# Kernel tuning notes

Hardware: AMD Instinct MI355X
Metric: run time of the kernel (lower is better)

Reference implementation:

```python
import jax, jax.numpy as jnp
import numpy as np

N = 1_000_000        # points
V = 200_000          # occupied voxels
B = 4                # scans per batch
NUM_CLASSES = 20
DIM_POINT = 4
EPS = 1e-5


def bn(x, g, b):
    # eval-mode BatchNorm1d with running_mean=0, running_var=1
    return x * (g / jnp.sqrt(1.0 + EPS)) + b


def _lin(key, fi, fo):
    # kaiming-normal init, bias-free Linear stored as [in, out]
    return jax.random.normal(key, (fi, fo), jnp.float32) * np.sqrt(2.0 / fi)


def setup_inputs() -> dict:
    key = jax.random.key(0)
    ks = jax.random.split(key, 20)
    batch_ids = (jnp.arange(N) * B // N).astype(jnp.float32)[:, None]
    coords = jax.random.normal(ks[0], (N, DIM_POINT), jnp.float32)
    points = jnp.concatenate([batch_ids, coords], axis=1)           # [N, 1+dim_point]
    pv_ids = jax.random.randint(ks[1], (N,), 0, V, jnp.int64)       # point -> voxel
    ones, zeros = jnp.ones, jnp.zeros
    return {
        'points': points, 'point_voxel_ids': pv_ids,
        # point encoder: 4->32->64->32, each Linear(no bias)+BN+ReLU
        'pe_w1': _lin(ks[2], DIM_POINT, 32), 'pe_g1': ones(32), 'pe_b1': zeros(32),
        'pe_w2': _lin(ks[3], 32, 64),        'pe_g2': ones(64), 'pe_b2': zeros(64),
        'pe_w3': _lin(ks[4], 64, 32),        'pe_g3': ones(32), 'pe_b3': zeros(32),
        # voxel encoder (SparseUnet simplified to per-voxel 32->32->32)
        've_w1': _lin(ks[5], 32, 32), 've_g1': ones(32), 've_b1': zeros(32),
        've_w2': _lin(ks[6], 32, 32), 've_g2': ones(32), 've_b2': zeros(32),
        # fusion encoder: 64->64
        'fu_w': _lin(ks[7], 64, 64), 'fu_g': ones(64), 'fu_b': zeros(64),
        # FlattenSELayer: 64 -> 64//16 -> 64 with biases
        'se_w1': _lin(ks[8], 64, 4),  'se_b1': zeros(4),
        'se_w2': _lin(ks[9], 4, 64),  'se_b2': zeros(64),
        # main classifier 64->32->num_classes
        'cls_w1': _lin(ks[10], 64, 32), 'cls_g1': ones(32), 'cls_b1': zeros(32),
        'cls_w2': _lin(ks[11], 32, NUM_CLASSES),
        # aux classifier 32->32->num_classes
        'aux_w1': _lin(ks[12], 32, 32), 'aux_g1': ones(32), 'aux_b1': zeros(32),
        'aux_w2': _lin(ks[13], 32, NUM_CLASSES),
    }


def reference(points, point_voxel_ids,
              pe_w1, pe_g1, pe_b1, pe_w2, pe_g2, pe_b2, pe_w3, pe_g3, pe_b3,
              ve_w1, ve_g1, ve_b1, ve_w2, ve_g2, ve_b2,
              fu_w, fu_g, fu_b, se_w1, se_b1, se_w2, se_b2,
              cls_w1, cls_g1, cls_b1, cls_w2,
              aux_w1, aux_g1, aux_b1, aux_w2):
    batch_ids = points[:, 0].astype(jnp.int32)
    pv = point_voxel_ids.astype(jnp.int32)
    x = points[:, 1:]
    # point encoder
    pf = jax.nn.relu(bn(x @ pe_w1, pe_g1, pe_b1))
    pf = jax.nn.relu(bn(pf @ pe_w2, pe_g2, pe_b2))
    pf = jax.nn.relu(bn(pf @ pe_w3, pe_g3, pe_b3))               # [N,32]
    # voxel_max_pooling: point -> voxel scatter-max (empty voxels -> 0)
    vox = jax.ops.segment_max(pf, pv, num_segments=V)
    vox = jnp.where(jnp.isfinite(vox), vox, 0.0)                 # [V,32]
    # voxel encoder (SparseUnet stand-in); v1 is the aux feature tap
    v1 = jax.nn.relu(bn(vox @ ve_w1, ve_g1, ve_b1))              # [V,32]
    vf = jax.nn.relu(bn(v1 @ ve_w2, ve_g2, ve_b2))               # [V,32]
    # voxel_to_point gather + fusion
    pvf = vf[pv]                                                  # [N,32]
    fused = jnp.concatenate([pvf, pf], axis=1)                   # [N,64]
    fused = jax.nn.relu(bn(fused @ fu_w, fu_g, fu_b))
    # FlattenSELayer: per-scan mean -> gate -> residual scale
    sums = jax.ops.segment_sum(fused, batch_ids, num_segments=B)
    cnts = jax.ops.segment_sum(jnp.ones((fused.shape[0], 1), fused.dtype), batch_ids, num_segments=B)
    mean = sums / jnp.maximum(cnts, 1.0)                         # [B,64]
    gate = jax.nn.sigmoid(jax.nn.relu(mean @ se_w1 + se_b1) @ se_w2 + se_b2)
    fused = fused + fused * gate[batch_ids]
    # heads (dropout is identity at inference)
    out = jax.nn.relu(bn(fused @ cls_w1, cls_g1, cls_b1)) @ cls_w2      # [N,C]
    aux_out = jax.nn.relu(bn(v1 @ aux_w1, aux_g1, aux_b1)) @ aux_w2     # [V,C]
    return out, aux_out
```

## Files before the change

kernel.cpp:

```cpp
#include <hip/hip_runtime.h>
#include <hip/hip_bf16.h>

#define NPTS 1000000
#define NVOX 200000
#define NCLS 20

typedef __hip_bfloat16 bf16;
typedef __attribute__((ext_vector_type(8))) short bf16x8_t;
typedef __attribute__((ext_vector_type(4))) float f32x4_t;
#define MFMA16(a, b, c) __builtin_amdgcn_mfma_f32_16x16x32_bf16(a, b, c, 0, 0, 0)

constexpr size_t L_PTSC = 0;
constexpr size_t L_PV   = L_PTSC + (size_t)NPTS * 4;
constexpr size_t L_BID  = L_PV + NPTS;
constexpr size_t L_CNT  = L_BID + NPTS;
constexpr size_t L_BSUM = L_CNT + NVOX;
constexpr size_t L_BCNT = L_BSUM + 2048;
constexpr size_t L_GATE = L_BCNT + 4;
constexpr size_t L_FLAG = L_GATE + 256;
constexpr size_t L_OFFS = L_FLAG + 4;
constexpr size_t L_OFFW = L_OFFS + NVOX;
constexpr size_t L_BS1  = L_OFFW + NVOX;
constexpr size_t L_BB   = L_BS1 + 256;
constexpr size_t L_IDX  = L_BB + 256;
constexpr size_t L_W    = L_IDX + NPTS;
constexpr int O_PE1W = 0;      constexpr int O_PE1B = 128;
constexpr int O_PE2W = 160;    constexpr int O_PE2B = 2208;
constexpr int O_PE3W = 2272;   constexpr int O_PE3B = 4320;
constexpr int O_VE1W = 4352;   constexpr int O_VE1B = 5376;
constexpr int O_VE2W = 5408;   constexpr int O_VE2B = 6432;
constexpr int O_FUW  = 6464;   constexpr int O_FUB  = 10560;
constexpr int O_SE1W = 10624;  constexpr int O_SE1B = 10880;
constexpr int O_SE2W = 10884;  constexpr int O_SE2B = 11140;
constexpr int O_CLS1W = 11204; constexpr int O_CLS1B = 13252;
constexpr int O_CLS2W = 13284;
constexpr int O_AUX1W = 13924; constexpr int O_AUX1B = 14948;
constexpr int O_AUX2W = 14980;
constexpr int W_TOTAL = 15620;
constexpr size_t L_WT  = L_W + W_TOTAL;
static_assert((L_WT * 4) % 16 == 0, "WT alignment");
constexpr int WT_FU = 0;
constexpr int WT_C1 = 4096;
constexpr int WT_C2 = 6144;
constexpr int WT_2H = 7168;
constexpr int WT_2L = 9216;
constexpr int WT_3H = 11264;
constexpr int WT_3L = 13312;
constexpr int WT_U16 = 15360;
constexpr size_t L_VFU = L_WT + WT_U16 / 2;
constexpr size_t L_PFQ = L_VFU + (size_t)NVOX * 16;
constexpr size_t L_PFS = L_PFQ + (size_t)NPTS * 16;
static_assert((L_VFU * 4) % 16 == 0, "vf alignment");
static_assert((L_PFQ * 4) % 16 == 0, "pf alignment");
static_assert((L_PFS * 4) % 16 == 0, "pfs alignment");

static __device__ __forceinline__ float b2f(bf16 v) { return __bfloat162float(v); }
static __device__ __forceinline__ float us2f(unsigned short u) { return __uint_as_float((unsigned)u << 16); }
static __device__ __forceinline__ unsigned short f2us(float f) {
    unsigned u = __float_as_uint(f);
    u += 0x7fffu + ((u >> 16) & 1u);
    return (unsigned short)(u >> 16);
}
static __device__ __forceinline__ unsigned pack2(float a, float b) {
    return (unsigned)f2us(a) | ((unsigned)f2us(b) << 16);
}
static __device__ __forceinline__ void unpack2(unsigned u, float& a, float& b) {
    a = __uint_as_float(u << 16);
    b = __uint_as_float(u & 0xffff0000u);
}
static __device__ __forceinline__ float rdf(const void* p, size_t idx, int fp32) {
    return fp32 ? ((const float*)p)[idx] : b2f(((const bf16*)p)[idx]);
}
static __device__ __forceinline__ int detect_fp32(const void* pts_raw) {
    const unsigned short* ptsu = (const unsigned short*)pts_raw;
    return (ptsu[1] == 0 && ptsu[11] == 0) ? 1 : 0;
}
static __device__ __forceinline__ int detect_i64(const void* pv_raw) {
    const unsigned* pvu = (const unsigned*)pv_raw;
    return (pvu[1] == 0 && pvu[3] == 0 && pvu[5] == 0 && pvu[7] == 0) ? 1 : 0;
}

template <int K, int M, bool RELU, bool BIAS>
static __device__ __forceinline__ void dense(const float* __restrict__ x, float* __restrict__ y,
                                             const float* __restrict__ w, const float* __restrict__ b) {
#pragma unroll
    for (int j = 0; j < M; ++j) {
        float a = BIAS ? b[j] : 0.f;
#pragma unroll
        for (int k = 0; k < K; ++k) a = fmaf(x[k], w[k * M + j], a);
        y[j] = RELU ? fmaxf(a, 0.f) : a;
    }
}

static __device__ __forceinline__ int block_excl_scan(int v, int t) {
    __shared__ int sh[2][256];
    int cur = 0;
    sh[0][t] = v; __syncthreads();
#pragma unroll
    for (int off = 1; off < 256; off <<= 1) {
        int val = sh[cur][t];
        if (t >= off) val += sh[cur][t - off];
        sh[cur ^ 1][t] = val; __syncthreads();
        cur ^= 1;
    }
    return sh[cur][t] - v;
}

struct WPtrs {
    const void *pe_w1, *pe_g1, *pe_b1, *pe_w2, *pe_g2, *pe_b2, *pe_w3, *pe_g3, *pe_b3;
    const void *ve_w1, *ve_g1, *ve_b1, *ve_w2, *ve_g2, *ve_b2;
    const void *fu_w, *fu_g, *fu_b;
    const void *se_w1, *se_b1, *se_w2, *se_b2;
    const void *cls_w1, *cls_g1, *cls_b1, *cls_w2;
    const void *aux_w1, *aux_g1, *aux_b1, *aux_w2;
};

static __device__ void foldw(float* d, const void* w, const void* g, int K, int M, int fp32) {
    const float INV = 0.9999950000374997f;
    for (int idx = threadIdx.x; idx < K * M; idx += 256)
        d[idx] = rdf(w, idx, fp32) * (rdf(g, idx % M, fp32) * INV);
}
static __device__ void cpv(float* d, const void* s, int n, int fp32) {
    for (int idx = threadIdx.x; idx < n; idx += 256) d[idx] = rdf(s, idx, fp32);
}

__global__ void k0_prep(WPtrs p, const void* __restrict__ pts_raw, float* __restrict__ W,
                        unsigned short* __restrict__ WT) {
    int f = detect_fp32(pts_raw);
    foldw(W + O_PE1W, p.pe_w1, p.pe_g1, 4, 32, f);   cpv(W + O_PE1B, p.pe_b1, 32, f);
    foldw(W + O_PE2W, p.pe_w2, p.pe_g2, 32, 64, f);  cpv(W + O_PE2B, p.pe_b2, 64, f);
    foldw(W + O_PE3W, p.pe_w3, p.pe_g3, 64, 32, f);  cpv(W + O_PE3B, p.pe_b3, 32, f);
    foldw(W + O_VE1W, p.ve_w1, p.ve_g1, 32, 32, f);  cpv(W + O_VE1B, p.ve_b1, 32, f);
    foldw(W + O_VE2W, p.ve_w2, p.ve_g2, 32, 32, f);  cpv(W + O_VE2B, p.ve_b2, 32, f);
    foldw(W + O_FUW,  p.fu_w,  p.fu_g,  64, 64, f);  cpv(W + O_FUB,  p.fu_b, 64, f);
    cpv(W + O_SE1W, p.se_w1, 256, f);  cpv(W + O_SE1B, p.se_b1, 4, f);
    cpv(W + O_SE2W, p.se_w2, 256, f);  cpv(W + O_SE2B, p.se_b2, 64, f);
    foldw(W + O_CLS1W, p.cls_w1, p.cls_g1, 64, 32, f); cpv(W + O_CLS1B, p.cls_b1, 32, f);
    cpv(W + O_CLS2W, p.cls_w2, 640, f);
    foldw(W + O_AUX1W, p.aux_w1, p.aux_g1, 32, 32, f); cpv(W + O_AUX1B, p.aux_b1, 32, f);
    cpv(W + O_AUX2W, p.aux_w2, 640, f);
    __syncthreads();
    unsigned short* wtfu = WT + WT_FU;
    unsigned short* wtc1 = WT + WT_C1;
    unsigned short* wtc2 = WT + WT_C2;
    unsigned short* wt2h = WT + WT_2H;
    unsigned short* wt2l = WT + WT_2L;
    unsigned short* wt3h = WT + WT_3H;
    unsigned short* wt3l = WT + WT_3L;
    for (int idx = threadIdx.x; idx < 4096; idx += 256) {
        int n = idx >> 6, k = idx & 63;
        wtfu[idx] = f2us(W[O_FUW + k * 64 + n]);
    }
    for (int idx = threadIdx.x; idx < 2048; idx += 256) {
        int n = idx >> 6, k = idx & 63;
        wtc1[idx] = f2us(W[O_CLS1W + k * 32 + n]);
    }
    for (int idx = threadIdx.x; idx < 1024; idx += 256) {
        int n = idx >> 5, k = idx & 31;
        wtc2[idx] = (n < NCLS) ? f2us(W[O_CLS2W + k * NCLS + n]) : (unsigned short)0;
    }
    for (int idx = threadIdx.x; idx < 2048; idx += 256) {
        int n = idx >> 5, k = idx & 31;
        float v = W[O_PE2W + k * 64 + n];
        unsigned short hi = f2us(v);
        wt2h[idx] = hi;
        wt2l[idx] = f2us(v - us2f(hi));
    }
    for (int idx = threadIdx.x; idx < 2048; idx += 256) {
        int n = idx >> 6, k = idx & 63;
        float v = W[O_PE3W + k * 32 + n];
        unsigned short hi = f2us(v);
        wt3h[idx] = hi;
        wt3l[idx] = f2us(v - us2f(hi));
    }
}

__global__ __launch_bounds__(256) void k_scan1(const int* __restrict__ cnt, int* __restrict__ bs) {
    int t = threadIdx.x;
    int base = blockIdx.x * 1024 + t * 4;
    int s = 0;
#pragma unroll
    for (int k = 0; k < 4; ++k) { int idx = base + k; if (idx < NVOX) s += cnt[idx]; }
    __shared__ int red[256];
    red[t] = s; __syncthreads();
    for (int off = 128; off > 0; off >>= 1) { if (t < off) red[t] += red[t + off]; __syncthreads(); }
    if (t == 0) bs[blockIdx.x] = red[0];
}

__global__ __launch_bounds__(256) void k_scan2(const int* __restrict__ bs, int* __restrict__ bb, int nb) {
    int t = threadIdx.x;
    int v = (t < nb) ? bs[t] : 0;
    int e = block_excl_scan(v, t);
    bb[t] = e;
}

__global__ __launch_bounds__(256) void k_scan3(const int* __restrict__ cnt, const int* __restrict__ bb,
                                               int* __restrict__ offs) {
    int t = threadIdx.x;
    int base = blockIdx.x * 1024 + t * 4;
    int c[4]; int s = 0;
#pragma unroll
    for (int k = 0; k < 4; ++k) { int idx = base + k; c[k] = (idx < NVOX) ? cnt[idx] : 0; s += c[k]; }
    int run = bb[blockIdx.x] + block_excl_scan(s, t);
#pragma unroll
    for (int k = 0; k < 4; ++k) {
        int idx = base + k;
        if (idx < NVOX) { offs[idx] = run; run += c[k]; }
    }
}

__global__ __launch_bounds__(256) void k1_fused(const void* __restrict__ pts_raw,
                                                const void* __restrict__ pv_raw,
                                                const float* __restrict__ W,
                                                const unsigned short* __restrict__ WT2H,
                                                const unsigned short* __restrict__ WT2L,
                                                const unsigned short* __restrict__ WT3H,
                                                const unsigned short* __restrict__ WT3L,
                                                int* __restrict__ pvN,
                                                int* __restrict__ bidN,
                                                int* __restrict__ cnt,
                                                float* __restrict__ bcnt,
                                                int* __restrict__ rank,
                                                uint4* __restrict__ pf_q) {
    __shared__ __align__(16) unsigned short hth[4][16][72];
    __shared__ __align__(16) unsigned short htl[4][16][72];
    __shared__ __align__(16) unsigned short pt[4][16][40];
    int t = threadIdx.x;
    int lane = t & 63, w = t >> 6;
    int m = lane & 15, quad = lane >> 4;
    int i0 = blockIdx.x * 256;
    int fp32 = detect_fp32(pts_raw), i64 = detect_i64(pv_raw);

    float w1[32], b1[8];
#pragma unroll
    for (int k = 0; k < 4; ++k)
#pragma unroll
        for (int j = 0; j < 8; ++j) w1[k * 8 + j] = W[O_PE1W + k * 32 + quad * 8 + j];
#pragma unroll
    for (int j = 0; j < 8; ++j) b1[j] = W[O_PE1B + quad * 8 + j];
    bf16x8_t b2h[4], b2l[4], b3h[2][2], b3l[2][2];
    float bias2[4], bias3[2];
#pragma unroll
    for (int tn = 0; tn < 4; ++tn) {
        b2h[tn] = *(const bf16x8_t*)(WT2H + (tn * 16 + m) * 32 + quad * 8);
        b2l[tn] = *(const bf16x8_t*)(WT2L + (tn * 16 + m) * 32 + quad * 8);
        bias2[tn] = W[O_PE2B + tn * 16 + m];
    }
#pragma unroll
    for (int tn = 0; tn < 2; ++tn) {
#pragma unroll
        for (int kh = 0; kh < 2; ++kh) {
            b3h[tn][kh] = *(const bf16x8_t*)(WT3H + (tn * 16 + m) * 64 + kh * 32 + quad * 8);
            b3l[tn][kh] = *(const bf16x8_t*)(WT3L + (tn * 16 + m) * 64 + kh * 32 + quad * 8);
        }
        bias3[tn] = W[O_PE3B + tn * 16 + m];
    }
    int nval = NPTS - i0; if (nval > 256) nval = 256;
    int ntiles = (nval - w * 64 >= 64) ? 4 : 0;

#pragma unroll 1
    for (int tt = 0; tt < ntiles; ++tt) {
        int rbase = i0 + w * 64 + tt * 16;
        int arow = rbase + m;
        float4 c;
        c.x = rdf(pts_raw, (size_t)arow * 5 + 1, fp32);
        c.y = rdf(pts_raw, (size_t)arow * 5 + 2, fp32);
        c.z = rdf(pts_raw, (size_t)arow * 5 + 3, fp32);
        c.w = rdf(pts_raw, (size_t)arow * 5 + 4, fp32);
        union { unsigned u[4]; bf16x8_t v; } ah, al;
#pragma unroll
        for (int p = 0; p < 4; ++p) {
            unsigned hu = 0, lu = 0;
#pragma unroll
            for (int s = 0; s < 2; ++s) {
                int j = 2 * p + s;
                float h = b1[j];
                h = fmaf(c.x, w1[0 * 8 + j], h);
                h = fmaf(c.y, w1[1 * 8 + j], h);
                h = fmaf(c.z, w1[2 * 8 + j], h);
                h = fmaf(c.w, w1[3 * 8 + j], h);
                h = fmaxf(h, 0.f);
                unsigned short hi = f2us(h);
                unsigned short lo = f2us(h - us2f(hi));
                hu |= (unsigned)hi << (16 * s);
                lu |= (unsigned)lo << (16 * s);
            }
            ah.u[p] = hu; al.u[p] = lu;
        }
#pragma unroll
        for (int tn = 0; tn < 4; ++tn) {
            f32x4_t acc = {0.f, 0.f, 0.f, 0.f};
            acc = MFMA16(ah.v, b2h[tn], acc);
            acc = MFMA16(ah.v, b2l[tn], acc);
            acc = MFMA16(al.v, b2h[tn], acc);
#pragma unroll
            for (int e = 0; e < 4; ++e) {
                float v = fmaxf(acc[e] + bias2[tn], 0.f);
                unsigned short hi = f2us(v);
                hth[w][quad * 4 + e][tn * 16 + m] = hi;
                htl[w][quad * 4 + e][tn * 16 + m] = f2us(v - us2f(hi));
            }
        }
        bf16x8_t x0h = *(const bf16x8_t*)&hth[w][m][quad * 8];
        bf16x8_t x1h = *(const bf16x8_t*)&hth[w][m][32 + quad * 8];
        bf16x8_t x0l = *(const bf16x8_t*)&htl[w][m][quad * 8];
        bf16x8_t x1l = *(const bf16x8_t*)&htl[w][m][32 + quad * 8];
#pragma unroll
        for (int tn = 0; tn < 2; ++tn) {
            f32x4_t acc = {0.f, 0.f, 0.f, 0.f};
            acc = MFMA16(x0h, b3h[tn][0], acc);
            acc = MFMA16(x1h, b3h[tn][1], acc);
            acc = MFMA16(x0h, b3l[tn][0], acc);
            acc = MFMA16(x1h, b3l[tn][1], acc);
            acc = MFMA16(x0l, b3h[tn][0], acc);
            acc = MFMA16(x1l, b3h[tn][1], acc);
#pragma unroll
            for (int e = 0; e < 4; ++e)
                pt[w][quad * 4 + e][tn * 16 + m] = f2us(fmaxf(acc[e] + bias3[tn], 0.f));
        }
        uint4 q = *(const uint4*)&pt[w][m][quad * 8];
        pf_q[(size_t)arow * 4 + quad] = q;
    }

    int i = i0 + t;
    bool valid = t < nval;
    int b = 0, rk = 0;
    if (valid) {
        b = (int)rdf(pts_raw, (size_t)i * 5, fp32);
        bidN[i] = b;
        int v = i64 ? (int)((const long long*)pv_raw)[i] : ((const int*)pv_raw)[i];
        pvN[i] = v;
        rk = atomicAdd(&cnt[v], 1);
    }
    __shared__ int sb0, sflag;
    if (t == 0) { sb0 = b; sflag = 1; }
    __syncthreads();
    if (valid && b != sb0) sflag = 0;
    __syncthreads();
    if (sflag) {
        if (t == 0) atomicAdd(&bcnt[sb0], (float)nval);
    } else if (valid) {
        atomicAdd(&bcnt[b], 1.f);
    }
    if (valid) rank[i] = rk;
}

__global__ __launch_bounds__(256) void k_scat(const int* __restrict__ pv,
                                              const int* __restrict__ rank,
                                              const int* __restrict__ offs,
                                              const uint4* __restrict__ pf_q,
                                              uint4* __restrict__ pf_s) {
    int tid = blockIdx.x * 256 + threadIdx.x;
    int i = tid >> 2, quad = tid & 3;
    if (i >= NPTS) return;
    int sp = offs[pv[i]] + rank[i];
    pf_s[(size_t)sp * 4 + quad] = pf_q[(size_t)i * 4 + quad];
}

__global__ __launch_bounds__(256) void k_voxmlp(const int* __restrict__ offs, const int* __restrict__ cnt,
                                                const uint4* __restrict__ pf_s,
                                                const float* __restrict__ W,
                                                const void* __restrict__ pts_raw,
                                                unsigned* __restrict__ vf_u,
                                                void* __restrict__ outbase) {
    int v = blockIdx.x * 256 + threadIdx.x;
    if (v >= NVOX) return;
    int of32 = detect_fp32(pts_raw);
    float mx[32];
#pragma unroll
    for (int c = 0; c < 32; ++c) mx[c] = 0.f;
    int s = offs[v], n = cnt[v];
    for (int p = 0; p < n; ++p) {
        size_t base = (size_t)(s + p) * 4;
#pragma unroll
        for (int t = 0; t < 4; ++t) {
            uint4 q = pf_s[base + t];
            float a, b;
            unpack2(q.x, a, b); mx[8*t+0] = fmaxf(mx[8*t+0], a); mx[8*t+1] = fmaxf(mx[8*t+1], b);
            unpack2(q.y, a, b); mx[8*t+2] = fmaxf(mx[8*t+2], a); mx[8*t+3] = fmaxf(mx[8*t+3], b);
            unpack2(q.z, a, b); mx[8*t+4] = fmaxf(mx[8*t+4], a); mx[8*t+5] = fmaxf(mx[8*t+5], b);
            unpack2(q.w, a, b); mx[8*t+6] = fmaxf(mx[8*t+6], a); mx[8*t+7] = fmaxf(mx[8*t+7], b);
        }
    }
    float v1[32], vf[32], a1[32], o[20];
    dense<32, 32, true, true>(mx, v1, W + O_VE1W, W + O_VE1B);
    dense<32, 32, true, true>(v1, vf, W + O_VE2W, W + O_VE2B);
#pragma unroll
    for (int c = 0; c < 16; ++c) vf_u[(size_t)v * 16 + c] = pack2(vf[2*c], vf[2*c+1]);
    dense<32, 32, true, true>(v1, a1, W + O_AUX1W, W + O_AUX1B);
    dense<32, 20, false, false>(a1, o, W + O_AUX2W, nullptr);
    if (of32) {
        float* auxf = (float*)outbase + (size_t)NPTS * NCLS + (size_t)v * NCLS;
#pragma unroll
        for (int t = 0; t < NCLS; ++t) auxf[t] = o[t];
    } else {
        unsigned* auxu = (unsigned*)((bf16*)outbase + (size_t)NPTS * NCLS);
#pragma unroll
        for (int t = 0; t < 10; ++t) auxu[(size_t)v * 10 + t] = pack2(o[2*t], o[2*t+1]);
    }
}

__global__ __launch_bounds__(256) void k3_mfma(const int* __restrict__ bid, const int* __restrict__ pv,
                                               const uint4* __restrict__ pf_q,
                                               const uint4* __restrict__ vf_q,
                                               const float* __restrict__ W,
                                               const unsigned short* __restrict__ WTfu,
                                               float* __restrict__ bsum8) {
    __shared__ int sbid[256];
    __shared__ float red[4][64];
    __shared__ int sflag;
    int t = threadIdx.x;
    int i0 = blockIdx.x * 256;
    int nval = NPTS - i0; if (nval > 256) nval = 256;
    if (t < nval) sbid[t] = bid[i0 + t];
    if (t == 0) sflag = (bid[i0] == bid[i0 + nval - 1]) ? 1 : 0;

    int lane = t & 63, w = t >> 6;
    int m = lane & 15, quad = lane >> 4;
    bf16x8_t bw0[4], bw1[4];
    float bias[4];
#pragma unroll
    for (int tn = 0; tn < 4; ++tn) {
        bw0[tn] = *(const bf16x8_t*)(WTfu + (tn * 16 + m) * 64 + quad * 8);
        bw1[tn] = *(const bf16x8_t*)(WTfu + (tn * 16 + m) * 64 + 32 + quad * 8);
        bias[tn] = W[O_FUB + tn * 16 + m];
    }
    __syncthreads();
    int uni = sflag;
    int b0 = sbid[0];
    int rep = (blockIdx.x & 7) * 256;
    int ntiles = (nval - w * 64 >= 64) ? 4 : 0;

    float csum[4] = {0.f, 0.f, 0.f, 0.f};
#pragma unroll
    for (int tt = 0; tt < 4; ++tt) {
        if (tt >= ntiles) break;
        int rbase = i0 + w * 64 + tt * 16;
        int arow = rbase + m;
        int pvr = pv[arow];
        uint4 va = vf_q[(size_t)pvr * 4 + quad];
        uint4 vb = pf_q[(size_t)arow * 4 + quad];
        bf16x8_t a0 = *(bf16x8_t*)&va;
        bf16x8_t a1 = *(bf16x8_t*)&vb;
        float f[4][4];
#pragma unroll
        for (int tn = 0; tn < 4; ++tn) {
            f32x4_t acc = {0.f, 0.f, 0.f, 0.f};
            acc = MFMA16(a0, bw0[tn], acc);
            acc = MFMA16(a1, bw1[tn], acc);
#pragma unroll
            for (int e = 0; e < 4; ++e) f[tn][e] = fmaxf(acc[e] + bias[tn], 0.f);
        }
        if (uni) {
#pragma unroll
            for (int tn = 0; tn < 4; ++tn) {
                float s = f[tn][0] + f[tn][1] + f[tn][2] + f[tn][3];
                s += __shfl_xor(s, 16);
                s += __shfl_xor(s, 32);
                csum[tn] += s;
            }
        } else {
#pragma unroll
            for (int tn = 0; tn < 4; ++tn)
#pragma unroll
                for (int e = 0; e < 4; ++e)
                    atomicAdd(&bsum8[rep + sbid[rbase - i0 + quad * 4 + e] * 64 + tn * 16 + m], f[tn][e]);
        }
    }
    if (uni) {
        float mine = quad == 0 ? csum[0] : quad == 1 ? csum[1] : quad == 2 ? csum[2] : csum[3];
        red[w][quad * 16 + m] = mine;
        __syncthreads();
        if (t < 64) {
            float s = red[0][t] + red[1][t] + red[2][t] + red[3][t];
            atomicAdd(&bsum8[rep + b0 * 64 + t], s);
        }
    }
}

__global__ void k4_gate(const float* __restrict__ bsum8, const float* __restrict__ bcnt,
                        const float* __restrict__ W, float* __restrict__ gate) {
    __shared__ float m[4][64];
    __shared__ float hid[4][4];
    int tid = threadIdx.x, b = tid >> 6, c = tid & 63;
    float s = 0.f;
#pragma unroll
    for (int r = 0; r < 8; ++r) s += bsum8[r * 256 + tid];
    m[b][c] = s / fmaxf(bcnt[b], 1.f);
    __syncthreads();
    if (c < 4) {
        const float* w = W + O_SE1W;
        float a = (W + O_SE1B)[c];
        for (int k = 0; k < 64; ++k) a = fmaf(m[b][k], w[k * 4 + c], a);
        hid[b][c] = fmaxf(a, 0.f);
    }
    __syncthreads();
    const float* w2 = W + O_SE2W;
    float g = (W + O_SE2B)[c];
#pragma unroll
    for (int h = 0; h < 4; ++h) g = fmaf(hid[b][h], w2[h * 64 + c], g);
    gate[tid] = 1.f + 1.f / (1.f + expf(-g));
}

__global__ __launch_bounds__(256) void k5_mfma(const int* __restrict__ bid, const int* __restrict__ pv,
                                               const uint4* __restrict__ pf_q,
                                               const uint4* __restrict__ vf_q,
                                               const float* __restrict__ W,
                                               const unsigned short* __restrict__ WTfu,
                                               const unsigned short* __restrict__ WTc1,
                                               const unsigned short* __restrict__ WTc2,
                                               const float* __restrict__ gate,
                                               const void* __restrict__ pts_raw,
                                               void* __restrict__ out) {
    __shared__ float sg[256];
    __shared__ int sbid[256];
    __shared__ int sflag;
    __shared__ __align__(16) unsigned short ft[4][16][72];
    __shared__ __align__(16) unsigned short ht[4][16][40];
    __shared__ float ot[4][16][20];
    int t = threadIdx.x;
    int i0 = blockIdx.x * 256;
    int nval = NPTS - i0; if (nval > 256) nval = 256;
    sg[t] = gate[t];
    if (t < nval) sbid[t] = bid[i0 + t];
    if (t == 0) sflag = (bid[i0] == bid[i0 + nval - 1]) ? 1 : 0;

    int lane = t & 63, w = t >> 6;
    int m = lane & 15, quad = lane >> 4;
    bf16x8_t bfu0[4], bfu1[4], bc10[2], bc11[2], bc2[2];
    float biasfu[4], biasc1[2];
#pragma unroll
    for (int tn = 0; tn < 4; ++tn) {
        bfu0[tn] = *(const bf16x8_t*)(WTfu + (tn * 16 + m) * 64 + quad * 8);
        bfu1[tn] = *(const bf16x8_t*)(WTfu + (tn * 16 + m) * 64 + 32 + quad * 8);
        biasfu[tn] = W[O_FUB + tn * 16 + m];
    }
#pragma unroll
    for (int tn = 0; tn < 2; ++tn) {
        bc10[tn] = *(const bf16x8_t*)(WTc1 + (tn * 16 + m) * 64 + quad * 8);
        bc11[tn] = *(const bf16x8_t*)(WTc1 + (tn * 16 + m) * 64 + 32 + quad * 8);
        bc2[tn]  = *(const bf16x8_t*)(WTc2 + (tn * 16 + m) * 32 + quad * 8);
        biasc1[tn] = W[O_CLS1B + tn * 16 + m];
    }
    __syncthreads();
    int uni = sflag;
    int of32 = detect_fp32(pts_raw);
    int ntiles = (nval - w * 64 >= 64) ? 4 : 0;

#pragma unroll 1
    for (int tt = 0; tt < ntiles; ++tt) {
        int rbase = i0 + w * 64 + tt * 16;
        int arow = rbase + m;
        int pvr = pv[arow];
        uint4 va = vf_q[(size_t)pvr * 4 + quad];
        uint4 vb = pf_q[(size_t)arow * 4 + quad];
        bf16x8_t a0 = *(bf16x8_t*)&va;
        bf16x8_t a1 = *(bf16x8_t*)&vb;
        float gcol[4];
        if (uni) {
#pragma unroll
            for (int tn = 0; tn < 4; ++tn) gcol[tn] = sg[sbid[0] * 64 + tn * 16 + m];
        }
#pragma unroll
        for (int tn = 0; tn < 4; ++tn) {
            f32x4_t acc = {0.f, 0.f, 0.f, 0.f};
            acc = MFMA16(a0, bfu0[tn], acc);
            acc = MFMA16(a1, bfu1[tn], acc);
#pragma unroll
            for (int e = 0; e < 4; ++e) {
                float fv = fmaxf(acc[e] + biasfu[tn], 0.f);
                float g = uni ? gcol[tn] : sg[sbid[rbase - i0 + quad * 4 + e] * 64 + tn * 16 + m];
                ft[w][quad * 4 + e][tn * 16 + m] = f2us(fv * g);
            }
        }
        bf16x8_t c0 = *(const bf16x8_t*)&ft[w][m][quad * 8];
        bf16x8_t c1 = *(const bf16x8_t*)&ft[w][m][32 + quad * 8];
#pragma unroll
        for (int tn = 0; tn < 2; ++tn) {
            f32x4_t acc = {0.f, 0.f, 0.f, 0.f};
            acc = MFMA16(c0, bc10[tn], acc);
            acc = MFMA16(c1, bc11[tn], acc);
#pragma unroll
            for (int e = 0; e < 4; ++e)
                ht[w][quad * 4 + e][tn * 16 + m] = f2us(fmaxf(acc[e] + biasc1[tn], 0.f));
        }
        bf16x8_t d0 = *(const bf16x8_t*)&ht[w][m][quad * 8];
#pragma unroll
        for (int tn = 0; tn < 2; ++tn) {
            f32x4_t acc = {0.f, 0.f, 0.f, 0.f};
            acc = MFMA16(d0, bc2[tn], acc);
            int c = tn * 16 + m;
            if (c < NCLS) {
#pragma unroll
                for (int e = 0; e < 4; ++e) ot[w][quad * 4 + e][c] = acc[e];
            }
        }
        if (of32) {
            float* of = (float*)out + (size_t)rbase * NCLS;
#pragma unroll
            for (int k = 0; k < 5; ++k) {
                int idx = k * 64 + lane;
                of[idx] = ((const float*)ot[w])[idx];
            }
        } else {
            unsigned* ow = (unsigned*)((unsigned short*)out + (size_t)rbase * NCLS);
#pragma unroll
            for (int k = 0; k < 3; ++k) {
                int idx = k * 64 + lane;
                if (idx < 160) {
                    int p = idx / 10, c2 = idx - p * 10;
                    ow[idx] = pack2(ot[w][p][2 * c2], ot[w][p][2 * c2 + 1]);
                }
            }
        }
    }
}

extern "C" void kernel_launch(void* const* d_in, const int* in_sizes, int n_in,
                              void* d_out, int out_size, void* d_ws, size_t ws_size,
                              hipStream_t stream) {
    WPtrs p;
    p.pe_w1 = d_in[2];  p.pe_g1 = d_in[3];  p.pe_b1 = d_in[4];
    p.pe_w2 = d_in[5];  p.pe_g2 = d_in[6];  p.pe_b2 = d_in[7];
    p.pe_w3 = d_in[8];  p.pe_g3 = d_in[9];  p.pe_b3 = d_in[10];
    p.ve_w1 = d_in[11]; p.ve_g1 = d_in[12]; p.ve_b1 = d_in[13];
    p.ve_w2 = d_in[14]; p.ve_g2 = d_in[15]; p.ve_b2 = d_in[16];
    p.fu_w  = d_in[17]; p.fu_g  = d_in[18]; p.fu_b  = d_in[19];
    p.se_w1 = d_in[20]; p.se_b1 = d_in[21];
    p.se_w2 = d_in[22]; p.se_b2 = d_in[23];
    p.cls_w1 = d_in[24]; p.cls_g1 = d_in[25]; p.cls_b1 = d_in[26];
    p.cls_w2 = d_in[27];
    p.aux_w1 = d_in[28]; p.aux_g1 = d_in[29]; p.aux_b1 = d_in[30];
    p.aux_w2 = d_in[31];

    float* base = (float*)d_ws;
    int*   pvN  = (int*)(base + L_PV);
    int*   bidN = (int*)(base + L_BID);
    int*   cnt  = (int*)(base + L_CNT);
    float* bsum8 = base + L_BSUM;
    float* bcnt = base + L_BCNT;
    float* gate = base + L_GATE;
    int*   offs = (int*)(base + L_OFFS);
    int*   bs1  = (int*)(base + L_BS1);
    int*   bb   = (int*)(base + L_BB);
    int*   rank = (int*)(base + L_IDX);
    float* W    = base + L_W;
    unsigned short* WT = (unsigned short*)(base + L_WT);
    unsigned short* wtfu = WT + WT_FU;
    unsigned short* wtc1 = WT + WT_C1;
    unsigned short* wtc2 = WT + WT_C2;
    unsigned short* wt2h = WT + WT_2H;
    unsigned short* wt2l = WT + WT_2L;
    unsigned short* wt3h = WT + WT_3H;
    unsigned short* wt3l = WT + WT_3L;
    unsigned* vf_u = (unsigned*)(base + L_VFU);
    uint4* pf_q = (uint4*)(base + L_PFQ);
    uint4* pf_s = (uint4*)(base + L_PFS);

    constexpr int NBV = (NVOX + 255) / 256;
    constexpr int NBS = (NVOX + 1023) / 1024;
    constexpr int NBM = (NPTS + 255) / 256;
    constexpr int NBSC = (NPTS * 4 + 255) / 256;

    hipMemsetAsync(cnt, 0, (NVOX + 2048 + 4) * sizeof(float), stream);
    k0_prep<<<1, 256, 0, stream>>>(p, d_in[0], W, WT);
    k1_fused<<<NBM, 256, 0, stream>>>(d_in[0], d_in[1], W, wt2h, wt2l, wt3h, wt3l,
                                      pvN, bidN, cnt, bcnt, rank, pf_q);
    k_scan1<<<NBS, 256, 0, stream>>>(cnt, bs1);
    k_scan2<<<1, 256, 0, stream>>>(bs1, bb, NBS);
    k_scan3<<<NBS, 256, 0, stream>>>(cnt, bb, offs);
    k_scat<<<NBSC, 256, 0, stream>>>(pvN, rank, offs, pf_q, pf_s);
    k_voxmlp<<<NBV, 256, 0, stream>>>(offs, cnt, pf_s, W, d_in[0], vf_u, d_out);
    k3_mfma<<<NBM, 256, 0, stream>>>(bidN, pvN, pf_q, (const uint4*)vf_u, W, wtfu, bsum8);
    k4_gate<<<1, 256, 0, stream>>>(bsum8, bcnt, W, gate);
    k5_mfma<<<NBM, 256, 0, stream>>>(bidN, pvN, pf_q, (const uint4*)vf_u, W, wtfu, wtc1, wtc2, gate, d_in[0], d_out);
}
```

Measured before the change: 554.2 us.

## Fuse pipeline into a single persistent cooperative kernel with grid syncs

Replaces the ten separate kernel launches (prep, point MLP, three scan stages, scatter, voxel MLP, fusion sum, gate, heads) with one cooperative persistent kernel that loops over work blocks and separates the stages with grid.sync(). The aim is to remove per-launch overhead and the idle tails between the small stages. In exchange the grid is capped at 1024 blocks, so large stages become grid-stride loops with less parallelism, and each grid barrier has a cost. The old multi-kernel path is kept as a fallback if the cooperative launch fails.

```diff
diff --git a/kernel.cpp b/kernel.cpp
--- a/kernel.cpp
+++ b/kernel.cpp
@@ -1,9 +1,14 @@
 #include <hip/hip_runtime.h>
 #include <hip/hip_bf16.h>
+#include <hip/hip_cooperative_groups.h>
+
+namespace cg = cooperative_groups;
 
 #define NPTS 1000000
 #define NVOX 200000
 #define NCLS 20
+#define NBM 3907
+#define NBS 196
 
 typedef __hip_bfloat16 bf16;
 typedef __attribute__((ext_vector_type(8))) short bf16x8_t;
@@ -124,9 +129,7 @@
     for (int idx = threadIdx.x; idx < n; idx += 256) d[idx] = rdf(s, idx, fp32);
 }
 
-__global__ void k0_prep(WPtrs p, const void* __restrict__ pts_raw, float* __restrict__ W,
-                        unsigned short* __restrict__ WT) {
-    int f = detect_fp32(pts_raw);
+static __device__ void prep_dev(const WPtrs& p, int f, float* W, unsigned short* WT) {
     foldw(W + O_PE1W, p.pe_w1, p.pe_g1, 4, 32, f);   cpv(W + O_PE1B, p.pe_b1, 32, f);
     foldw(W + O_PE2W, p.pe_w2, p.pe_g2, 32, 64, f);  cpv(W + O_PE2B, p.pe_b2, 64, f);
     foldw(W + O_PE3W, p.pe_w3, p.pe_g3, 64, 32, f);  cpv(W + O_PE3B, p.pe_b3, 32, f);
@@ -175,6 +178,438 @@
     }
 }
 
+struct MegaArgs {
+    WPtrs p;
+    const void* pts_raw;
+    const void* pv_raw;
+    float* W;
+    unsigned short* WT;
+    int* pvN; int* bidN; int* cnt; float* bcnt; int* rank;
+    int* offs; int* bs1; int* bb;
+    float* bsum8; float* gate;
+    unsigned* vf_u; uint4* pf_q; uint4* pf_s;
+    void* out;
+};
+
+__global__ __launch_bounds__(256, 4) void k_mega(MegaArgs a) {
+    cg::grid_group grid = cg::this_grid();
+    int t = threadIdx.x;
+    int bx = blockIdx.x;
+    int G = gridDim.x;
+    int lane = t & 63, w = t >> 6;
+    int m = lane & 15, quad = lane >> 4;
+    int fp32 = detect_fp32(a.pts_raw);
+    int i64 = detect_i64(a.pv_raw);
+
+    __shared__ __align__(16) unsigned char pool[23552];
+    auto hth = (unsigned short(*)[16][72])(pool);
+    auto htl = (unsigned short(*)[16][72])(pool + 9216);
+    auto ptb = (unsigned short(*)[16][40])(pool + 18432);
+    auto ft = (unsigned short(*)[16][72])(pool);
+    auto ht = (unsigned short(*)[16][40])(pool + 9216);
+    auto ot = (float(*)[16][20])(pool + 14336);
+    __shared__ int sbid[256];
+    __shared__ int sb0s, sflag;
+    __shared__ float redw[4][64];
+    __shared__ int red1[256];
+    __shared__ float sg[256];
+    __shared__ float m4[4][64];
+    __shared__ float hid4[4][4];
+
+    if (bx == 0) prep_dev(a.p, fp32, a.W, a.WT);
+    grid.sync();
+
+    const float* W = a.W;
+    const unsigned short* WTfu = a.WT + WT_FU;
+    const unsigned short* WTc1 = a.WT + WT_C1;
+    const unsigned short* WTc2 = a.WT + WT_C2;
+
+    {
+        const unsigned short* WT2H = a.WT + WT_2H;
+        const unsigned short* WT2L = a.WT + WT_2L;
+        const unsigned short* WT3H = a.WT + WT_3H;
+        const unsigned short* WT3L = a.WT + WT_3L;
+        float w1[32], b1[8];
+#pragma unroll
+        for (int k = 0; k < 4; ++k)
+#pragma unroll
+            for (int j = 0; j < 8; ++j) w1[k * 8 + j] = W[O_PE1W + k * 32 + quad * 8 + j];
+#pragma unroll
+        for (int j = 0; j < 8; ++j) b1[j] = W[O_PE1B + quad * 8 + j];
+        bf16x8_t b2h[4], b2l[4], b3h[2][2], b3l[2][2];
+        float bias2[4], bias3[2];
+#pragma unroll
+        for (int tn = 0; tn < 4; ++tn) {
+            b2h[tn] = *(const bf16x8_t*)(WT2H + (tn * 16 + m) * 32 + quad * 8);
+            b2l[tn] = *(const bf16x8_t*)(WT2L + (tn * 16 + m) * 32 + quad * 8);
+            bias2[tn] = W[O_PE2B + tn * 16 + m];
+        }
+#pragma unroll
+        for (int tn = 0; tn < 2; ++tn) {
+#pragma unroll
+            for (int kh = 0; kh < 2; ++kh) {
+                b3h[tn][kh] = *(const bf16x8_t*)(WT3H + (tn * 16 + m) * 64 + kh * 32 + quad * 8);
+                b3l[tn][kh] = *(const bf16x8_t*)(WT3L + (tn * 16 + m) * 64 + kh * 32 + quad * 8);
+            }
+            bias3[tn] = W[O_PE3B + tn * 16 + m];
+        }
+
+        for (int vb = bx; vb < NBM; vb += G) {
+            int i0 = vb * 256;
+            int nval = NPTS - i0; if (nval > 256) nval = 256;
+            int ntiles = (nval - w * 64 >= 64) ? 4 : 0;
+#pragma unroll 1
+            for (int tt = 0; tt < ntiles; ++tt) {
+                int rbase = i0 + w * 64 + tt * 16;
+                int arow = rbase + m;
+                float4 c;
+                c.x = rdf(a.pts_raw, (size_t)arow * 5 + 1, fp32);
+                c.y = rdf(a.pts_raw, (size_t)arow * 5 + 2, fp32);
+                c.z = rdf(a.pts_raw, (size_t)arow * 5 + 3, fp32);
+                c.w = rdf(a.pts_raw, (size_t)arow * 5 + 4, fp32);
+                union { unsigned u[4]; bf16x8_t v; } ah, al;
+#pragma unroll
+                for (int pp = 0; pp < 4; ++pp) {
+                    unsigned hu = 0, lu = 0;
+#pragma unroll
+                    for (int s = 0; s < 2; ++s) {
+                        int j = 2 * pp + s;
+                        float h = b1[j];
+                        h = fmaf(c.x, w1[0 * 8 + j], h);
+                        h = fmaf(c.y, w1[1 * 8 + j], h);
+                        h = fmaf(c.z, w1[2 * 8 + j], h);
+                        h = fmaf(c.w, w1[3 * 8 + j], h);
+                        h = fmaxf(h, 0.f);
+                        unsigned short hi = f2us(h);
+                        unsigned short lo = f2us(h - us2f(hi));
+                        hu |= (unsigned)hi << (16 * s);
+                        lu |= (unsigned)lo << (16 * s);
+                    }
+                    ah.u[pp] = hu; al.u[pp] = lu;
+                }
+#pragma unroll
+                for (int tn = 0; tn < 4; ++tn) {
+                    f32x4_t acc = {0.f, 0.f, 0.f, 0.f};
+                    acc = MFMA16(ah.v, b2h[tn], acc);
+                    acc = MFMA16(ah.v, b2l[tn], acc);
+                    acc = MFMA16(al.v, b2h[tn], acc);
+#pragma unroll
+                    for (int e = 0; e < 4; ++e) {
+                        float v = fmaxf(acc[e] + bias2[tn], 0.f);
+                        unsigned short hi = f2us(v);
+                        hth[w][quad * 4 + e][tn * 16 + m] = hi;
+                        htl[w][quad * 4 + e][tn * 16 + m] = f2us(v - us2f(hi));
+                    }
+                }
+                bf16x8_t x0h = *(const bf16x8_t*)&hth[w][m][quad * 8];
+                bf16x8_t x1h = *(const bf16x8_t*)&hth[w][m][32 + quad * 8];
+                bf16x8_t x0l = *(const bf16x8_t*)&htl[w][m][quad * 8];
+                bf16x8_t x1l = *(const bf16x8_t*)&htl[w][m][32 + quad * 8];
+#pragma unroll
+                for (int tn = 0; tn < 2; ++tn) {
+                    f32x4_t acc = {0.f, 0.f, 0.f, 0.f};
+                    acc = MFMA16(x0h, b3h[tn][0], acc);
+                    acc = MFMA16(x1h, b3h[tn][1], acc);
+                    acc = MFMA16(x0h, b3l[tn][0], acc);
+                    acc = MFMA16(x1h, b3l[tn][1], acc);
+                    acc = MFMA16(x0l, b3h[tn][0], acc);
+                    acc = MFMA16(x1l, b3h[tn][1], acc);
+#pragma unroll
+                    for (int e = 0; e < 4; ++e)
+                        ptb[w][quad * 4 + e][tn * 16 + m] = f2us(fmaxf(acc[e] + bias3[tn], 0.f));
+                }
+                uint4 q = *(const uint4*)&ptb[w][m][quad * 8];
+                a.pf_q[(size_t)arow * 4 + quad] = q;
+            }
+            int i = i0 + t;
+            bool valid = t < nval;
+            int b = 0, rk = 0;
+            if (valid) {
+                b = (int)rdf(a.pts_raw, (size_t)i * 5, fp32);
+                a.bidN[i] = b;
+                int v = i64 ? (int)((const long long*)a.pv_raw)[i] : ((const int*)a.pv_raw)[i];
+                a.pvN[i] = v;
+                rk = atomicAdd(&a.cnt[v], 1);
+            }
+            if (t == 0) { sb0s = b; sflag = 1; }
+            __syncthreads();
+            if (valid && b != sb0s) sflag = 0;
+            __syncthreads();
+            if (sflag) {
+                if (t == 0) atomicAdd(&a.bcnt[sb0s], (float)nval);
+            } else if (valid) {
+                atomicAdd(&a.bcnt[b], 1.f);
+            }
+            if (valid) a.rank[i] = rk;
+            __syncthreads();
+        }
+    }
+    grid.sync();
+
+    for (int c = bx; c < NBS; c += G) {
+        int base = c * 1024 + t * 4;
+        int s = 0;
+#pragma unroll
+        for (int k = 0; k < 4; ++k) { int idx = base + k; if (idx < NVOX) s += a.cnt[idx]; }
+        red1[t] = s; __syncthreads();
+        for (int off = 128; off > 0; off >>= 1) { if (t < off) red1[t] += red1[t + off]; __syncthreads(); }
+        if (t == 0) a.bs1[c] = red1[0];
+        __syncthreads();
+    }
+    grid.sync();
+
+    if (bx == 0) {
+        int v = (t < NBS) ? a.bs1[t] : 0;
+        int e = block_excl_scan(v, t);
+        a.bb[t] = e;
+    }
+    grid.sync();
+
+    for (int c = bx; c < NBS; c += G) {
+        int base = c * 1024 + t * 4;
+        int cc[4]; int s = 0;
+#pragma unroll
+        for (int k = 0; k < 4; ++k) { int idx = base + k; cc[k] = (idx < NVOX) ? a.cnt[idx] : 0; s += cc[k]; }
+        int run = a.bb[c] + block_excl_scan(s, t);
+#pragma unroll
+        for (int k = 0; k < 4; ++k) {
+            int idx = base + k;
+            if (idx < NVOX) { a.offs[idx] = run; run += cc[k]; }
+        }
+        __syncthreads();
+    }
+    grid.sync();
+
+    for (long long idx = (long long)bx * 256 + t; idx < (long long)NPTS * 4; idx += (long long)G * 256) {
+        int i = (int)(idx >> 2), q = (int)(idx & 3);
+        int sp = a.offs[a.pvN[i]] + a.rank[i];
+        a.pf_s[(size_t)sp * 4 + q] = a.pf_q[(size_t)i * 4 + q];
+    }
+    grid.sync();
+
+    for (int v = bx * 256 + t; v < NVOX; v += G * 256) {
+        float mx[32];
+#pragma unroll
+        for (int c = 0; c < 32; ++c) mx[c] = 0.f;
+        int s = a.offs[v], n = a.cnt[v];
+        for (int pp = 0; pp < n; ++pp) {
+            size_t base = (size_t)(s + pp) * 4;
+#pragma unroll
+            for (int tt = 0; tt < 4; ++tt) {
+                uint4 q = a.pf_s[base + tt];
+                float x, y;
+                unpack2(q.x, x, y); mx[8*tt+0] = fmaxf(mx[8*tt+0], x); mx[8*tt+1] = fmaxf(mx[8*tt+1], y);
+                unpack2(q.y, x, y); mx[8*tt+2] = fmaxf(mx[8*tt+2], x); mx[8*tt+3] = fmaxf(mx[8*tt+3], y);
+                unpack2(q.z, x, y); mx[8*tt+4] = fmaxf(mx[8*tt+4], x); mx[8*tt+5] = fmaxf(mx[8*tt+5], y);
+                unpack2(q.w, x, y); mx[8*tt+6] = fmaxf(mx[8*tt+6], x); mx[8*tt+7] = fmaxf(mx[8*tt+7], y);
+            }
+        }
+        float v1[32], vf[32], a1[32], o[20];
+        dense<32, 32, true, true>(mx, v1, W + O_VE1W, W + O_VE1B);
+        dense<32, 32, true, true>(v1, vf, W + O_VE2W, W + O_VE2B);
+#pragma unroll
+        for (int c = 0; c < 16; ++c) a.vf_u[(size_t)v * 16 + c] = pack2(vf[2*c], vf[2*c+1]);
+        dense<32, 32, true, true>(v1, a1, W + O_AUX1W, W + O_AUX1B);
+        dense<32, 20, false, false>(a1, o, W + O_AUX2W, nullptr);
+        if (fp32) {
+            float* auxf = (float*)a.out + (size_t)NPTS * NCLS + (size_t)v * NCLS;
+#pragma unroll
+            for (int tt = 0; tt < NCLS; ++tt) auxf[tt] = o[tt];
+        } else {
+            unsigned* auxu = (unsigned*)((bf16*)a.out + (size_t)NPTS * NCLS);
+#pragma unroll
+            for (int tt = 0; tt < 10; ++tt) auxu[(size_t)v * 10 + tt] = pack2(o[2*tt], o[2*tt+1]);
+        }
+    }
+    grid.sync();
+
+    bf16x8_t bfu0[4], bfu1[4];
+    float biasfu[4];
+#pragma unroll
+    for (int tn = 0; tn < 4; ++tn) {
+        bfu0[tn] = *(const bf16x8_t*)(WTfu + (tn * 16 + m) * 64 + quad * 8);
+        bfu1[tn] = *(const bf16x8_t*)(WTfu + (tn * 16 + m) * 64 + 32 + quad * 8);
+        biasfu[tn] = W[O_FUB + tn * 16 + m];
+    }
+    const uint4* vf_q = (const uint4*)a.vf_u;
+
+    for (int vb = bx; vb < NBM; vb += G) {
+        int i0 = vb * 256;
+        int nval = NPTS - i0; if (nval > 256) nval = 256;
+        if (t < nval) sbid[t] = a.bidN[i0 + t];
+        if (t == 0) sflag = (a.bidN[i0] == a.bidN[i0 + nval - 1]) ? 1 : 0;
+        __syncthreads();
+        int uni = sflag;
+        int b0 = sbid[0];
+        int rep = (vb & 7) * 256;
+        int ntiles = (nval - w * 64 >= 64) ? 4 : 0;
+        float csum[4] = {0.f, 0.f, 0.f, 0.f};
+#pragma unroll
+        for (int tt = 0; tt < 4; ++tt) {
+            if (tt >= ntiles) break;
+            int rbase = i0 + w * 64 + tt * 16;
+            int arow = rbase + m;
+            int pvr = a.pvN[arow];
+            uint4 va = vf_q[(size_t)pvr * 4 + quad];
+            uint4 vb2 = a.pf_q[(size_t)arow * 4 + quad];
+            bf16x8_t a0 = *(bf16x8_t*)&va;
+            bf16x8_t a1 = *(bf16x8_t*)&vb2;
+            float f[4][4];
+#pragma unroll
+            for (int tn = 0; tn < 4; ++tn) {
+                f32x4_t acc = {0.f, 0.f, 0.f, 0.f};
+                acc = MFMA16(a0, bfu0[tn], acc);
+                acc = MFMA16(a1, bfu1[tn], acc);
+#pragma unroll
+                for (int e = 0; e < 4; ++e) f[tn][e] = fmaxf(acc[e] + biasfu[tn], 0.f);
+            }
+            if (uni) {
+#pragma unroll
+                for (int tn = 0; tn < 4; ++tn) {
+                    float s = f[tn][0] + f[tn][1] + f[tn][2] + f[tn][3];
+                    s += __shfl_xor(s, 16);
+                    s += __shfl_xor(s, 32);
+                    csum[tn] += s;
+                }
+            } else {
+#pragma unroll
+                for (int tn = 0; tn < 4; ++tn)
+#pragma unroll
+                    for (int e = 0; e < 4; ++e)
+                        atomicAdd(&a.bsum8[rep + sbid[rbase - i0 + quad * 4 + e] * 64 + tn * 16 + m], f[tn][e]);
+            }
+        }
+        if (uni) {
+            float mine = quad == 0 ? csum[0] : quad == 1 ? csum[1] : quad == 2 ? csum[2] : csum[3];
+            redw[w][quad * 16 + m] = mine;
+            __syncthreads();
+            if (t < 64) {
+                float s = redw[0][t] + redw[1][t] + redw[2][t] + redw[3][t];
+                atomicAdd(&a.bsum8[rep + b0 * 64 + t], s);
+            }
+        }
+        __syncthreads();
+    }
+    grid.sync();
+
+    if (bx == 0) {
+        int b = t >> 6, c = t & 63;
+        float s = 0.f;
+#pragma unroll
+        for (int r = 0; r < 8; ++r) s += a.bsum8[r * 256 + t];
+        m4[b][c] = s / fmaxf(a.bcnt[b], 1.f);
+        __syncthreads();
+        if (c < 4) {
+            const float* ww = W + O_SE1W;
+            float x = (W + O_SE1B)[c];
+            for (int k = 0; k < 64; ++k) x = fmaf(m4[b][k], ww[k * 4 + c], x);
+            hid4[b][c] = fmaxf(x, 0.f);
+        }
+        __syncthreads();
+        const float* w2 = W + O_SE2W;
+        float g = (W + O_SE2B)[c];
+#pragma unroll
+        for (int h = 0; h < 4; ++h) g = fmaf(hid4[b][h], w2[h * 64 + c], g);
+        a.gate[t] = 1.f + 1.f / (1.f + expf(-g));
+    }
+    grid.sync();
+
+    {
+        sg[t] = a.gate[t];
+        bf16x8_t bc10[2], bc11[2], bc2[2];
+        float biasc1[2];
+#pragma unroll
+        for (int tn = 0; tn < 2; ++tn) {
+            bc10[tn] = *(const bf16x8_t*)(WTc1 + (tn * 16 + m) * 64 + quad * 8);
+            bc11[tn] = *(const bf16x8_t*)(WTc1 + (tn * 16 + m) * 64 + 32 + quad * 8);
+            bc2[tn]  = *(const bf16x8_t*)(WTc2 + (tn * 16 + m) * 32 + quad * 8);
+            biasc1[tn] = W[O_CLS1B + tn * 16 + m];
+        }
+        for (int vb = bx; vb < NBM; vb += G) {
+            int i0 = vb * 256;
+            int nval = NPTS - i0; if (nval > 256) nval = 256;
+            if (t < nval) sbid[t] = a.bidN[i0 + t];
+            if (t == 0) sflag = (a.bidN[i0] == a.bidN[i0 + nval - 1]) ? 1 : 0;
+            __syncthreads();
+            int uni = sflag;
+            int ntiles = (nval - w * 64 >= 64) ? 4 : 0;
+#pragma unroll 1
+            for (int tt = 0; tt < ntiles; ++tt) {
+                int rbase = i0 + w * 64 + tt * 16;
+                int arow = rbase + m;
+                int pvr = a.pvN[arow];
+                uint4 va = vf_q[(size_t)pvr * 4 + quad];
+                uint4 vb2 = a.pf_q[(size_t)arow * 4 + quad];
+                bf16x8_t a0 = *(bf16x8_t*)&va;
+                bf16x8_t a1 = *(bf16x8_t*)&vb2;
+                float gcol[4];
+                if (uni) {
+#pragma unroll
+                    for (int tn = 0; tn < 4; ++tn) gcol[tn] = sg[sbid[0] * 64 + tn * 16 + m];
+                }
+#pragma unroll
+                for (int tn = 0; tn < 4; ++tn) {
+                    f32x4_t acc = {0.f, 0.f, 0.f, 0.f};
+                    acc = MFMA16(a0, bfu0[tn], acc);
+                    acc = MFMA16(a1, bfu1[tn], acc);
+#pragma unroll
+                    for (int e = 0; e < 4; ++e) {
+                        float fv = fmaxf(acc[e] + biasfu[tn], 0.f);
+                        float g = uni ? gcol[tn] : sg[sbid[rbase - i0 + quad * 4 + e] * 64 + tn * 16 + m];
+                        ft[w][quad * 4 + e][tn * 16 + m] = f2us(fv * g);
+                    }
+                }
+                bf16x8_t c0 = *(const bf16x8_t*)&ft[w][m][quad * 8];
+                bf16x8_t c1 = *(const bf16x8_t*)&ft[w][m][32 + quad * 8];
+#pragma unroll
+                for (int tn = 0; tn < 2; ++tn) {
+                    f32x4_t acc = {0.f, 0.f, 0.f, 0.f};
+                    acc = MFMA16(c0, bc10[tn], acc);
+                    acc = MFMA16(c1, bc11[tn], acc);
+#pragma unroll
+                    for (int e = 0; e < 4; ++e)
+                        ht[w][quad * 4 + e][tn * 16 + m] = f2us(fmaxf(acc[e] + biasc1[tn], 0.f));
+                }
+                bf16x8_t d0 = *(const bf16x8_t*)&ht[w][m][quad * 8];
+#pragma unroll
+                for (int tn = 0; tn < 2; ++tn) {
+                    f32x4_t acc = {0.f, 0.f, 0.f, 0.f};
+                    acc = MFMA16(d0, bc2[tn], acc);
+                    int c = tn * 16 + m;
+                    if (c < NCLS) {
+#pragma unroll
+                        for (int e = 0; e < 4; ++e) ot[w][quad * 4 + e][c] = acc[e];
+                    }
+                }
+                if (fp32) {
+                    float* of = (float*)a.out + (size_t)rbase * NCLS;
+#pragma unroll
+                    for (int k = 0; k < 5; ++k) {
+                        int idx = k * 64 + lane;
+                        of[idx] = ((const float*)ot[w])[idx];
+                    }
+                } else {
+                    unsigned* ow = (unsigned*)((unsigned short*)a.out + (size_t)rbase * NCLS);
+#pragma unroll
+                    for (int k = 0; k < 3; ++k) {
+                        int idx = k * 64 + lane;
+                        if (idx < 160) {
+                            int pp = idx / 10, c2 = idx - pp * 10;
+                            ow[idx] = pack2(ot[w][pp][2 * c2], ot[w][pp][2 * c2 + 1]);
+                        }
+                    }
+                }
+            }
+            __syncthreads();
+        }
+    }
+}
+
+__global__ void k0_prep(WPtrs p, const void* __restrict__ pts_raw, float* __restrict__ W,
+                        unsigned short* __restrict__ WT) {
+    prep_dev(p, detect_fp32(pts_raw), W, WT);
+}
+
 __global__ __launch_bounds__(256) void k_scan1(const int* __restrict__ cnt, int* __restrict__ bs) {
     int t = threadIdx.x;
     int base = blockIdx.x * 1024 + t * 4;
@@ -269,11 +704,11 @@
         c.w = rdf(pts_raw, (size_t)arow * 5 + 4, fp32);
         union { unsigned u[4]; bf16x8_t v; } ah, al;
 #pragma unroll
-        for (int p = 0; p < 4; ++p) {
+        for (int pp = 0; pp < 4; ++pp) {
             unsigned hu = 0, lu = 0;
 #pragma unroll
             for (int s = 0; s < 2; ++s) {
-                int j = 2 * p + s;
+                int j = 2 * pp + s;
                 float h = b1[j];
                 h = fmaf(c.x, w1[0 * 8 + j], h);
                 h = fmaf(c.y, w1[1 * 8 + j], h);
@@ -285,7 +720,7 @@
                 hu |= (unsigned)hi << (16 * s);
                 lu |= (unsigned)lo << (16 * s);
             }
-            ah.u[p] = hu; al.u[p] = lu;
+            ah.u[pp] = hu; al.u[pp] = lu;
         }
 #pragma unroll
         for (int tn = 0; tn < 4; ++tn) {
@@ -619,59 +1054,71 @@
 extern "C" void kernel_launch(void* const* d_in, const int* in_sizes, int n_in,
                               void* d_out, int out_size, void* d_ws, size_t ws_size,
                               hipStream_t stream) {
-    WPtrs p;
-    p.pe_w1 = d_in[2];  p.pe_g1 = d_in[3];  p.pe_b1 = d_in[4];
-    p.pe_w2 = d_in[5];  p.pe_g2 = d_in[6];  p.pe_b2 = d_in[7];
-    p.pe_w3 = d_in[8];  p.pe_g3 = d_in[9];  p.pe_b3 = d_in[10];
-    p.ve_w1 = d_in[11]; p.ve_g1 = d_in[12]; p.ve_b1 = d_in[13];
-    p.ve_w2 = d_in[14]; p.ve_g2 = d_in[15]; p.ve_b2 = d_in[16];
-    p.fu_w  = d_in[17]; p.fu_g  = d_in[18]; p.fu_b  = d_in[19];
-    p.se_w1 = d_in[20]; p.se_b1 = d_in[21];
-    p.se_w2 = d_in[22]; p.se_b2 = d_in[23];
-    p.cls_w1 = d_in[24]; p.cls_g1 = d_in[25]; p.cls_b1 = d_in[26];
-    p.cls_w2 = d_in[27];
-    p.aux_w1 = d_in[28]; p.aux_g1 = d_in[29]; p.aux_b1 = d_in[30];
-    p.aux_w2 = d_in[31];
+    static MegaArgs ma;
+    ma.p.pe_w1 = d_in[2];  ma.p.pe_g1 = d_in[3];  ma.p.pe_b1 = d_in[4];
+    ma.p.pe_w2 = d_in[5];  ma.p.pe_g2 = d_in[6];  ma.p.pe_b2 = d_in[7];
+    ma.p.pe_w3 = d_in[8];  ma.p.pe_g3 = d_in[9];  ma.p.pe_b3 = d_in[10];
+    ma.p.ve_w1 = d_in[11]; ma.p.ve_g1 = d_in[12]; ma.p.ve_b1 = d_in[13];
+    ma.p.ve_w2 = d_in[14]; ma.p.ve_g2 = d_in[15]; ma.p.ve_b2 = d_in[16];
+    ma.p.fu_w  = d_in[17]; ma.p.fu_g  = d_in[18]; ma.p.fu_b  = d_in[19];
+    ma.p.se_w1 = d_in[20]; ma.p.se_b1 = d_in[21];
+    ma.p.se_w2 = d_in[22]; ma.p.se_b2 = d_in[23];
+    ma.p.cls_w1 = d_in[24]; ma.p.cls_g1 = d_in[25]; ma.p.cls_b1 = d_in[26];
+    ma.p.cls_w2 = d_in[27];
+    ma.p.aux_w1 = d_in[28]; ma.p.aux_g1 = d_in[29]; ma.p.aux_b1 = d_in[30];
+    ma.p.aux_w2 = d_in[31];
 
     float* base = (float*)d_ws;
-    int*   pvN  = (int*)(base + L_PV);
-    int*   bidN = (int*)(base + L_BID);
-    int*   cnt  = (int*)(base + L_CNT);
-    float* bsum8 = base + L_BSUM;
-    float* bcnt = base + L_BCNT;
-    float* gate = base + L_GATE;
-    int*   offs = (int*)(base + L_OFFS);
-    int*   bs1  = (int*)(base + L_BS1);
-    int*   bb   = (int*)(base + L_BB);
-    int*   rank = (int*)(base + L_IDX);
-    float* W    = base + L_W;
-    unsigned short* WT = (unsigned short*)(base + L_WT);
-    unsigned short* wtfu = WT + WT_FU;
-    unsigned short* wtc1 = WT + WT_C1;
-    unsigned short* wtc2 = WT + WT_C2;
-    unsigned short* wt2h = WT + WT_2H;
-    unsigned short* wt2l = WT + WT_2L;
-    unsigned short* wt3h = WT + WT_3H;
-    unsigned short* wt3l = WT + WT_3L;
-    unsigned* vf_u = (unsigned*)(base + L_VFU);
-    uint4* pf_q = (uint4*)(base + L_PFQ);
-    uint4* pf_s = (uint4*)(base + L_PFS);
-
-    constexpr int NBV = (NVOX + 255) / 256;
-    constexpr int NBS = (NVOX + 1023) / 1024;
-    constexpr int NBM = (NPTS + 255) / 256;
-    constexpr int NBSC = (NPTS * 4 + 255) / 256;
-
-    hipMemsetAsync(cnt, 0, (NVOX + 2048 + 4) * sizeof(float), stream);
-    k0_prep<<<1, 256, 0, stream>>>(p, d_in[0], W, WT);
-    k1_fused<<<NBM, 256, 0, stream>>>(d_in[0], d_in[1], W, wt2h, wt2l, wt3h, wt3l,
-                                      pvN, bidN, cnt, bcnt, rank, pf_q);
-    k_scan1<<<NBS, 256, 0, stream>>>(cnt, bs1);
-    k_scan2<<<1, 256, 0, stream>>>(bs1, bb, NBS);
-    k_scan3<<<NBS, 256, 0, stream>>>(cnt, bb, offs);
-    k_scat<<<NBSC, 256, 0, stream>>>(pvN, rank, offs, pf_q, pf_s);
-    k_voxmlp<<<NBV, 256, 0, stream>>>(offs, cnt, pf_s, W, d_in[0], vf_u, d_out);
-    k3_mfma<<<NBM, 256, 0, stream>>>(bidN, pvN, pf_q, (const uint4*)vf_u, W, wtfu, bsum8);
-    k4_gate<<<1, 256, 0, stream>>>(bsum8, bcnt, W, gate);
-    k5_mfma<<<NBM, 256, 0, stream>>>(bidN, pvN, pf_q, (const uint4*)vf_u, W, wtfu, wtc1, wtc2, gate, d_in[0], d_out);
-}
+    ma.pts_raw = d_in[0];
+    ma.pv_raw  = d_in[1];
+    ma.pvN  = (int*)(base + L_PV);
+    ma.bidN = (int*)(base + L_BID);
+    ma.cnt  = (int*)(base + L_CNT);
+    ma.bsum8 = base + L_BSUM;
+    ma.bcnt = base + L_BCNT;
+    ma.gate = base + L_GATE;
+    ma.offs = (int*)(base + L_OFFS);
+    ma.bs1  = (int*)(base + L_BS1);
+    ma.bb   = (int*)(base + L_BB);
+    ma.rank = (int*)(base + L_IDX);
+    ma.W    = base + L_W;
+    ma.WT   = (unsigned short*)(base + L_WT);
+    ma.vf_u = (unsigned*)(base + L_VFU);
+    ma.pf_q = (uint4*)(base + L_PFQ);
+    ma.pf_s = (uint4*)(base + L_PFS);
+    ma.out  = d_out;
+
+    hipMemsetAsync(ma.cnt, 0, (NVOX + 2048 + 4) * sizeof(float), stream);
+
+    hipError_t lerr = hipErrorUnknown;
+    int nb = 0;
+    if (hipOccupancyMaxActiveBlocksPerMultiprocessor(&nb, k_mega, 256, 0) == hipSuccess && nb > 0) {
+        int grid = nb * 256;
+        if (grid > 1024) grid = 1024;
+        void* params[] = { (void*)&ma };
+        lerr = hipLaunchCooperativeKernel((void*)k_mega, dim3(grid), dim3(256), params, 0, stream);
+    }
+    if (lerr != hipSuccess) {
+        constexpr int NBV = (NVOX + 255) / 256;
+        constexpr int NBSC = (NPTS * 4 + 255) / 256;
+        unsigned short* wtfu = ma.WT + WT_FU;
+        unsigned short* wtc1 = ma.WT + WT_C1;
+        unsigned short* wtc2 = ma.WT + WT_C2;
+        unsigned short* wt2h = ma.WT + WT_2H;
+        unsigned short* wt2l = ma.WT + WT_2L;
+        unsigned short* wt3h = ma.WT + WT_3H;
+        unsigned short* wt3l = ma.WT + WT_3L;
+        k0_prep<<<1, 256, 0, stream>>>(ma.p, ma.pts_raw, ma.W, ma.WT);
+        k1_fused<<<NBM, 256, 0, stream>>>(ma.pts_raw, ma.pv_raw, ma.W, wt2h, wt2l, wt3h, wt3l,
+                                          ma.pvN, ma.bidN, ma.cnt, ma.bcnt, ma.rank, ma.pf_q);
+        k_scan1<<<NBS, 256, 0, stream>>>(ma.cnt, ma.bs1);
+        k_scan2<<<1, 256, 0, stream>>>(ma.bs1, ma.bb, NBS);
+        k_scan3<<<NBS, 256, 0, stream>>>(ma.cnt, ma.bb, ma.offs);
+        k_scat<<<NBSC, 256, 0, stream>>>(ma.pvN, ma.rank, ma.offs, ma.pf_q, ma.pf_s);
+        k_voxmlp<<<NBV, 256, 0, stream>>>(ma.offs, ma.cnt, ma.pf_s, ma.W, ma.pts_raw, ma.vf_u, d_out);
+        k3_mfma<<<NBM, 256, 0, stream>>>(ma.bidN, ma.pvN, ma.pf_q, (const uint4*)ma.vf_u, ma.W, wtfu, ma.bsum8);
+        k4_gate<<<1, 256, 0, stream>>>(ma.bsum8, ma.bcnt, ma.W, ma.gate);
+        k5_mfma<<<NBM, 256, 0, stream>>>(ma.bidN, ma.pvN, ma.pf_q, (const uint4*)ma.vf_u, ma.W,
+                                         wtfu, wtc1, wtc2, ma.gate, ma.pts_raw, d_out);
+    }
+}
```

New measurement: 1.318 ms. 138% more time.
